# Optimization experiments

Measured on AMD Instinct MI355X. Metric: run time of the kernel, lower is better.

Reference implementation:

```python
import jax, jax.numpy as jnp
import numpy as np

B, H, W = 8, 56, 56
DIM_IN = 1792 + 2   # concatenated pyramid channels + 2 coord channels
D_OUT = 1792 // 4   # gamma_d = 4
N_CENTERS = H * W   # gamma_c = 1
K = 3


def avg_pool3(x):
    # F.avg_pool2d(x, 3, 1, 1) with count_include_pad=True: padded sum / 9
    s = jax.lax.reduce_window(x, 0.0, jax.lax.add, (1, 1, 3, 3), (1, 1, 1, 1),
                              ((0, 0), (0, 0), (1, 1), (1, 1)))
    return s / 9.0


def setup_inputs() -> dict:
    key = jax.random.key(0)
    k0, k1, k2, kw, kb, kc = jax.random.split(key, 6)
    p0 = jax.random.normal(k0, (B, 256, H, W), dtype=jnp.float32)
    p1 = jax.random.normal(k1, (B, 512, 28, 28), dtype=jnp.float32)
    p2 = jax.random.normal(k2, (B, 1024, 14, 14), dtype=jnp.float32)
    conv_w = jax.random.normal(kw, (D_OUT, DIM_IN), dtype=jnp.float32) * 0.02
    conv_b = jax.random.normal(kb, (D_OUT,), dtype=jnp.float32) * 0.01
    C = jax.random.normal(kc, (D_OUT, N_CENTERS), dtype=jnp.float32) * 0.5
    return {"p0": p0, "p1": p1, "p2": p2, "conv_w": conv_w, "conv_b": conv_b, "C": C}


def reference(p0, p1, p2, conv_w, conv_b, C):
    # Descriptor: avg-pool each level, upsample to first level, concat channels
    o0 = avg_pool3(p0)
    o1 = avg_pool3(p1)
    o2 = avg_pool3(p2)
    o1 = jax.image.resize(o1, (B, o1.shape[1], H, W), method='bilinear')  # align_corners=False equiv (upsample)
    o2 = jax.image.resize(o2, (B, o2.shape[1], H, W), method='bilinear')
    sample = jnp.concatenate([o0, o1, o2], axis=1)  # (B, 1792, H, W)

    # AddCoords: xx = row index / (H-1), yy = col index / (W-1), both *2-1
    xx = (jnp.arange(H, dtype=jnp.float32) / (H - 1) * 2 - 1)[:, None] * jnp.ones((1, W), jnp.float32)
    yy = (jnp.arange(W, dtype=jnp.float32) / (W - 1) * 2 - 1)[None, :] * jnp.ones((H, 1), jnp.float32)
    coords = jnp.broadcast_to(jnp.stack([xx, yy])[None], (B, 2, H, W))
    sample = jnp.concatenate([sample, coords], axis=1)  # (B, 1794, H, W)

    # 1x1 CoordConv
    phi = jnp.einsum('bchw,oc->bohw', sample, conv_w) + conv_b[None, :, None, None]
    phi_p = phi.transpose(0, 2, 3, 1).reshape(B, H * W, D_OUT)  # b (h w) c

    # squared distance to center bank via norm expansion
    feat2 = jnp.sum(phi_p ** 2, axis=2, keepdims=True)        # (B, HW, 1)
    cent2 = jnp.sum(C ** 2, axis=0)[None, None, :]            # (1, 1, N)
    dist = jnp.sqrt(feat2 + cent2 - 2.0 * jnp.matmul(phi_p, C))  # (B, HW, N)

    # top-K smallest, ascending
    neg_top, _ = jax.lax.top_k(-dist, K)
    topv = -neg_top                                           # (B, HW, K) ascending
    soft = jax.nn.softmax(-topv, axis=-1)                     # softmin
    score = soft[:, :, 0] * topv[:, :, 0]                     # (B, HW)
    return score.reshape(B, 1, H, W)
```

## Files before the change

kernel.cpp:

```cpp
#include <hip/hip_runtime.h>
#include <math.h>

#define B_    8
#define H_    56
#define W_    56
#define HW_   3136
#define C0_   256
#define C1_   512
#define C2_   1024
#define DIN_  1794
#define KD_   1792
#define KCP_  56
#define DOUT_ 448
#define NCHP_ 28
#define NC_   3136
#define NCHD_ 196
#define KCD_  14
#define DTS_  452
#define PCH_  28672

typedef __attribute__((ext_vector_type(8))) short bh8;
typedef __attribute__((ext_vector_type(4))) float f32x4;

__device__ __forceinline__ short f2bf(float f) {
  union { float f; unsigned u; } v; v.f = f;
  unsigned r = v.u + 0x7fffu + ((v.u >> 16) & 1u);
  return (short)(r >> 16);
}
__device__ __forceinline__ float bf2f(short s) {
  union { unsigned u; float f; } v; v.u = ((unsigned)(unsigned short)s) << 16;
  return v.f;
}

__global__ __launch_bounds__(256) void desc0_kernel(const float* __restrict__ p0,
                                                    short* __restrict__ desc) {
  __shared__ float sv[64 * 57];
  const int c0 = blockIdx.x * 64, h = blockIdx.y, b = blockIdx.z;
  for (int item = threadIdx.x; item < 64 * 56; item += 256) {
    int x = item % 56, c = item / 56;
    const float* src = p0 + (((size_t)(b * C0_ + c0 + c)) * 56 + h) * 56 + x;
    float s = src[0];
    if (h > 0)  s += src[-56];
    if (h < 55) s += src[56];
    sv[c * 57 + x] = s;
  }
  __syncthreads();
  for (int item = threadIdx.x; item < 56 * 8; item += 256) {
    int g = item & 7, w = item >> 3;
    bh8 o;
#pragma unroll
    for (int j = 0; j < 8; ++j) {
      const float* s0 = sv + (g * 8 + j) * 57;
      float v = s0[w];
      if (w > 0)  v += s0[w - 1];
      if (w < 55) v += s0[w + 1];
      o[j] = f2bf(v * (1.0f / 9.0f));
    }
    size_t pid = (size_t)b * HW_ + h * 56 + w;
    *(bh8*)(desc + pid * KD_ + c0 + g * 8) = o;
  }
}

__global__ __launch_bounds__(256) void desc1_kernel(const float* __restrict__ p1,
                                                    short* __restrict__ desc) {
  __shared__ float sv[2 * 64 * 29];
  const int c0 = blockIdx.x * 64, h = blockIdx.y, b = blockIdx.z;
  float sy = (h + 0.5f) * 0.5f - 0.5f;
  float fyf = floorf(sy);
  float fy = sy - fyf;
  int iy = (int)fyf;
  int pya = min(max(iy, 0), 27), pyb = min(max(iy + 1, 0), 27);
  for (int item = threadIdx.x; item < 64 * 2 * 28; item += 256) {
    int x = item % 28;
    int pr = (item / 28) & 1;
    int c = item / 56;
    int r = pr ? pyb : pya;
    const float* src = p1 + (((size_t)(b * C1_ + c0 + c)) * 28 + r) * 28 + x;
    float s = src[0];
    if (r > 0)  s += src[-28];
    if (r < 27) s += src[28];
    sv[pr * (64 * 29) + c * 29 + x] = s;
  }
  __syncthreads();
  for (int item = threadIdx.x; item < 56 * 8; item += 256) {
    int g = item & 7, w = item >> 3;
    float sx = (w + 0.5f) * 0.5f - 0.5f;
    float fxf = floorf(sx);
    float fx = sx - fxf;
    int ix = (int)fxf;
    int x0 = min(max(ix, 0), 27), x1 = min(max(ix + 1, 0), 27);
    bh8 o;
#pragma unroll
    for (int j = 0; j < 8; ++j) {
      const float* s0 = sv + (g * 8 + j) * 29;
      const float* s1 = s0 + 64 * 29;
      float p00 = s0[x0] + (x0 > 0 ? s0[x0 - 1] : 0.f) + (x0 < 27 ? s0[x0 + 1] : 0.f);
      float p01 = s0[x1] + (x1 > 0 ? s0[x1 - 1] : 0.f) + (x1 < 27 ? s0[x1 + 1] : 0.f);
      float p10 = s1[x0] + (x0 > 0 ? s1[x0 - 1] : 0.f) + (x0 < 27 ? s1[x0 + 1] : 0.f);
      float p11 = s1[x1] + (x1 > 0 ? s1[x1 - 1] : 0.f) + (x1 < 27 ? s1[x1 + 1] : 0.f);
      float top = p00 + fx * (p01 - p00);
      float bot = p10 + fx * (p11 - p10);
      o[j] = f2bf((top + fy * (bot - top)) * (1.0f / 9.0f));
    }
    size_t pid = (size_t)b * HW_ + h * 56 + w;
    *(bh8*)(desc + pid * KD_ + C0_ + c0 + g * 8) = o;
  }
}

__global__ __launch_bounds__(256) void desc2_kernel(const float* __restrict__ p2,
                                                    short* __restrict__ desc) {
  __shared__ float sv[2 * 64 * 15];
  const int c0 = blockIdx.x * 64, h = blockIdx.y, b = blockIdx.z;
  float sy = (h + 0.5f) * 0.25f - 0.5f;
  float fyf = floorf(sy);
  float fy = sy - fyf;
  int iy = (int)fyf;
  int pya = min(max(iy, 0), 13), pyb = min(max(iy + 1, 0), 13);
  for (int item = threadIdx.x; item < 64 * 2 * 14; item += 256) {
    int x = item % 14;
    int pr = (item / 14) & 1;
    int c = item / 28;
    int r = pr ? pyb : pya;
    const float* src = p2 + (((size_t)(b * C2_ + c0 + c)) * 14 + r) * 14 + x;
    float s = src[0];
    if (r > 0)  s += src[-14];
    if (r < 13) s += src[14];
    sv[pr * (64 * 15) + c * 15 + x] = s;
  }
  __syncthreads();
  for (int item = threadIdx.x; item < 56 * 8; item += 256) {
    int g = item & 7, w = item >> 3;
    float sx = (w + 0.5f) * 0.25f - 0.5f;
    float fxf = floorf(sx);
    float fx = sx - fxf;
    int ix = (int)fxf;
    int x0 = min(max(ix, 0), 13), x1 = min(max(ix + 1, 0), 13);
    bh8 o;
#pragma unroll
    for (int j = 0; j < 8; ++j) {
      const float* s0 = sv + (g * 8 + j) * 15;
      const float* s1 = s0 + 64 * 15;
      float p00 = s0[x0] + (x0 > 0 ? s0[x0 - 1] : 0.f) + (x0 < 13 ? s0[x0 + 1] : 0.f);
      float p01 = s0[x1] + (x1 > 0 ? s0[x1 - 1] : 0.f) + (x1 < 13 ? s0[x1 + 1] : 0.f);
      float p10 = s1[x0] + (x0 > 0 ? s1[x0 - 1] : 0.f) + (x0 < 13 ? s1[x0 + 1] : 0.f);
      float p11 = s1[x1] + (x1 > 0 ? s1[x1 - 1] : 0.f) + (x1 < 13 ? s1[x1 + 1] : 0.f);
      float top = p00 + fx * (p01 - p00);
      float bot = p10 + fx * (p11 - p10);
      o[j] = f2bf((top + fy * (bot - top)) * (1.0f / 9.0f));
    }
    size_t pid = (size_t)b * HW_ + h * 56 + w;
    *(bh8*)(desc + pid * KD_ + C0_ + C1_ + c0 + g * 8) = o;
  }
}

__global__ void cent2_kernel(const float* __restrict__ C, float* __restrict__ c2) {
  int j = blockIdx.x * blockDim.x + threadIdx.x;
  if (j >= NC_) return;
  float s = 0.f;
  for (int d = 0; d < DOUT_; ++d) {
    float v = bf2f(f2bf(C[(size_t)d * NC_ + j]));
    s = fmaf(v, v, s);
  }
  c2[j] = s;
}

__global__ void cpack_kernel(const float* __restrict__ C, short* __restrict__ Cpk) {
  int idx = blockIdx.x * 256 + threadIdx.x;
  int ln = idx & 63;
  int kc = (idx >> 6) % KCD_;
  int nc = idx / (KCD_ * 64);
  int n  = nc * 16 + (ln & 15);
  int k0 = kc * 32 + ((ln >> 4) << 3);
  bh8 o;
#pragma unroll
  for (int j = 0; j < 8; ++j) o[j] = f2bf(C[(size_t)(k0 + j) * NC_ + n]);
  *(bh8*)(Cpk + (size_t)idx * 8) = o;
}

__global__ void wpack_kernel(const float* __restrict__ W, short* __restrict__ Wpk) {
  int idx = blockIdx.x * 256 + threadIdx.x;
  int ln = idx & 63;
  int kc = (idx >> 6) % KCP_;
  int nc = idx / (KCP_ * 64);
  int n  = nc * 16 + (ln & 15);
  int k0 = kc * 32 + ((ln >> 4) << 3);
  bh8 o;
#pragma unroll
  for (int j = 0; j < 8; ++j) o[j] = f2bf(W[(size_t)n * DIN_ + k0 + j]);
  *(bh8*)(Wpk + (size_t)idx * 8) = o;
}

__global__ __launch_bounds__(256) void phi_mfma(
    const short* __restrict__ desc, const short* __restrict__ Wpk,
    const float* __restrict__ cw, const float* __restrict__ cb,
    short* __restrict__ phip ) {
  __shared__ __align__(16) float Dt[16 * DTS_];
  const int wv = threadIdx.x >> 6, ln = threadIdx.x & 63;
  const int pix0 = blockIdx.x * 32;
  const short* aptr = desc + ((size_t)(pix0 + (ln & 15))) * KD_ + ((ln >> 4) << 3);

  f32x4 acc[2][7];
#pragma unroll
  for (int rc = 0; rc < 2; ++rc)
#pragma unroll
    for (int i = 0; i < 7; ++i) acc[rc][i] = (f32x4){0.f, 0.f, 0.f, 0.f};

  const short* bbase = Wpk + (size_t)(wv * 7) * (KCP_ * 512) + ln * 8;
  for (int kc = 0; kc < KCP_; ++kc) {
    bh8 a0 = *(const bh8*)(aptr + kc * 32);
    bh8 a1 = *(const bh8*)(aptr + 16 * KD_ + kc * 32);
    const short* bp = bbase + kc * 512;
#pragma unroll
    for (int i = 0; i < 7; ++i) {
      bh8 bfr = *(const bh8*)(bp + (size_t)i * (KCP_ * 512));
      acc[0][i] = __builtin_amdgcn_mfma_f32_16x16x32_bf16(a0, bfr, acc[0][i], 0, 0, 0);
      acc[1][i] = __builtin_amdgcn_mfma_f32_16x16x32_bf16(a1, bfr, acc[1][i], 0, 0, 0);
    }
  }

  for (int rc = 0; rc < 2; ++rc) {
    __syncthreads();
#pragma unroll
    for (int i = 0; i < 7; ++i) {
      int col = (wv * 7 + i) * 16 + (ln & 15);
      float bias = cb[col];
      float wx = cw[(size_t)col * DIN_ + 1792];
      float wy = cw[(size_t)col * DIN_ + 1793];
#pragma unroll
      for (int r = 0; r < 4; ++r) {
        int row = ((ln >> 4) << 2) + r;
        int pid = pix0 + rc * 16 + row;
        int hw = pid % HW_;
        int hh = hw / 56, ww = hw % 56;
        float xx = (float)hh * (2.0f / 55.0f) - 1.0f;
        float yy = (float)ww * (2.0f / 55.0f) - 1.0f;
        Dt[row * DTS_ + col] = acc[rc][i][r] + bias + wx * xx + wy * yy;
      }
    }
    __syncthreads();
    short* op = phip + (size_t)(blockIdx.x * 2 + rc) * PCH_;
    for (int item = threadIdx.x; item < KCD_ * 64; item += 256) {
      int kc = item >> 6, lp = item & 63;
      int m = lp & 15, k0 = kc * 32 + ((lp >> 4) << 3);
      bh8 o;
#pragma unroll
      for (int j = 0; j < 8; ++j) o[j] = f2bf(Dt[m * DTS_ + k0 + j]);
      *(bh8*)(op + (size_t)item * 8) = o;
    }
  }
}

__device__ __forceinline__ void insert3(float& t0, float& t1, float& t2, float v) {
  if (v < t2) {
    if (v < t1) {
      t2 = t1;
      if (v < t0) { t1 = t0; t0 = v; } else t1 = v;
    } else t2 = v;
  }
}
__device__ __forceinline__ void merge3(float& a0, float& a1, float& a2,
                                       float b0, float b1, float b2) {
  float lo0 = fminf(a0, b0), hi0 = fmaxf(a0, b0);
  float lo1 = fminf(a1, b1), hi1 = fmaxf(a1, b1);
  float lo2 = fminf(a2, b2);
  a0 = lo0;
  a1 = fminf(hi0, lo1);
  a2 = fminf(fmaxf(hi0, lo1), fminf(hi1, lo2));
}
__device__ __forceinline__ float sumsq8(bh8 a, float s) {
#pragma unroll
  for (int j = 0; j < 8; ++j) { float v = bf2f(a[j]); s = fmaf(v, v, s); }
  return s;
}

#define AFRAG_LIST(X) X(0) X(1) X(2) X(3) X(4) X(5) X(6) X(7) X(8) X(9) X(10) X(11) X(12) X(13)

__global__ __launch_bounds__(256, 2) void dist_part(
    const short* __restrict__ phip, const short* __restrict__ Cpk,
    const float* __restrict__ c2g, float* __restrict__ part) {
  __shared__ __align__(16) short Bst[2][14336];
  __shared__ float c2l[NC_ / 2];
  const int wv = threadIdx.x >> 6, ln = threadIdx.x & 63;
  const int half = blockIdx.x & 1;
  const int chunk = (blockIdx.x >> 1) * 4 + wv;

  for (int i = threadIdx.x; i < NC_ / 2; i += 256) c2l[i] = c2g[half * (NC_ / 2) + i];

  const short* ap = phip + (size_t)chunk * PCH_ + ln * 8;
#define LOADA(i) bh8 A##i = *(const bh8*)(ap + (i) * 512);
  AFRAG_LIST(LOADA)
#undef LOADA

  float sum = 0.f;
#define SQ(i) sum = sumsq8(A##i, sum);
  AFRAG_LIST(SQ)
#undef SQ
  sum += __shfl_xor(sum, 16, 64);
  sum += __shfl_xor(sum, 32, 64);
  const int rb = (ln >> 4) << 2;
  float f2r0 = __shfl(sum, rb + 0, 64);
  float f2r1 = __shfl(sum, rb + 1, 64);
  float f2r2 = __shfl(sum, rb + 2, 64);
  float f2r3 = __shfl(sum, rb + 3, 64);

  float t00 = 1e30f, t01 = 1e30f, t02 = 1e30f;
  float t10 = 1e30f, t11 = 1e30f, t12 = 1e30f;
  float t20 = 1e30f, t21 = 1e30f, t22 = 1e30f;
  float t30 = 1e30f, t31 = 1e30f, t32 = 1e30f;

  const int col = ln & 15;
  const short* cbase = Cpk + (size_t)half * ((NCHD_ / 2) * KCD_ * 512);

#define STAGE(buf, t) { \
    const short* g_ = cbase + (size_t)(t) * 14336 + wv * 3584 + ln * 8; \
    short* l_ = &Bst[(buf)][wv * 3584]; \
    _Pragma("unroll") \
    for (int j_ = 0; j_ < 7; ++j_) \
      __builtin_amdgcn_global_load_lds( \
          (const __attribute__((address_space(1))) unsigned int*)(g_ + j_ * 512), \
          (__attribute__((address_space(3))) unsigned int*)(l_ + j_ * 512), \
          16, 0, 0); }

  STAGE(0, 0)
  __syncthreads();

  for (int t = 0; t < NCHD_ / 4; ++t) {
    if (t < NCHD_ / 4 - 1) STAGE((t + 1) & 1, t + 1)
    const short* bp = &Bst[t & 1][ln * 8];
    f32x4 accA = {0.f, 0.f, 0.f, 0.f}, accB = {0.f, 0.f, 0.f, 0.f};
#define MF(kc) { \
    bh8 bA = *(const bh8*)(bp + (kc) * 512); \
    bh8 bB = *(const bh8*)(bp + 7168 + (kc) * 512); \
    accA = __builtin_amdgcn_mfma_f32_16x16x32_bf16(A##kc, bA, accA, 0, 0, 0); \
    accB = __builtin_amdgcn_mfma_f32_16x16x32_bf16(A##kc, bB, accB, 0, 0, 0); }
    AFRAG_LIST(MF)
#undef MF
    float c2A = c2l[t * 32 + col];
    float c2B = c2l[t * 32 + 16 + col];
    insert3(t00, t01, t02, f2r0 + c2A - 2.0f * accA[0]);
    insert3(t10, t11, t12, f2r1 + c2A - 2.0f * accA[1]);
    insert3(t20, t21, t22, f2r2 + c2A - 2.0f * accA[2]);
    insert3(t30, t31, t32, f2r3 + c2A - 2.0f * accA[3]);
    insert3(t00, t01, t02, f2r0 + c2B - 2.0f * accB[0]);
    insert3(t10, t11, t12, f2r1 + c2B - 2.0f * accB[1]);
    insert3(t20, t21, t22, f2r2 + c2B - 2.0f * accB[2]);
    insert3(t30, t31, t32, f2r3 + c2B - 2.0f * accB[3]);
    __syncthreads();
  }
#undef STAGE

#pragma unroll
  for (int m = 1; m <= 8; m <<= 1) {
    float b0, b1, b2;
    b0 = __shfl_xor(t00, m, 64); b1 = __shfl_xor(t01, m, 64); b2 = __shfl_xor(t02, m, 64);
    merge3(t00, t01, t02, b0, b1, b2);
    b0 = __shfl_xor(t10, m, 64); b1 = __shfl_xor(t11, m, 64); b2 = __shfl_xor(t12, m, 64);
    merge3(t10, t11, t12, b0, b1, b2);
    b0 = __shfl_xor(t20, m, 64); b1 = __shfl_xor(t21, m, 64); b2 = __shfl_xor(t22, m, 64);
    merge3(t20, t21, t22, b0, b1, b2);
    b0 = __shfl_xor(t30, m, 64); b1 = __shfl_xor(t31, m, 64); b2 = __shfl_xor(t32, m, 64);
    merge3(t30, t31, t32, b0, b1, b2);
  }

  if ((ln & 15) == 0) {
    float* q = part + ((size_t)(chunk * 16 + rb)) * 8 + half * 4;
    q[0] = t00; q[1] = t01; q[2] = t02;
    q[8] = t10; q[9] = t11; q[10] = t12;
    q[16] = t20; q[17] = t21; q[18] = t22;
    q[24] = t30; q[25] = t31; q[26] = t32;
  }
}

__global__ __launch_bounds__(256) void merge_kernel(const float* __restrict__ part,
                                                    float* __restrict__ out) {
  int p = blockIdx.x * 256 + threadIdx.x;
  const float* q = part + (size_t)p * 8;
  float a0 = q[0], a1 = q[1], a2 = q[2];
  merge3(a0, a1, a2, q[4], q[5], q[6]);
  float d0 = sqrtf(fmaxf(a0, 0.f));
  float d1 = sqrtf(fmaxf(a1, 0.f));
  float d2 = sqrtf(fmaxf(a2, 0.f));
  float s0 = 1.0f / (1.0f + expf(d0 - d1) + expf(d0 - d2));
  out[p] = s0 * d0;
}

extern "C" void kernel_launch(void* const* d_in, const int* in_sizes, int n_in,
                              void* d_out, int out_size, void* d_ws, size_t ws_size,
                              hipStream_t stream) {
  const float* p0 = (const float*)d_in[0];
  const float* p1 = (const float*)d_in[1];
  const float* p2 = (const float*)d_in[2];
  const float* cw = (const float*)d_in[3];
  const float* cb = (const float*)d_in[4];
  const float* C  = (const float*)d_in[5];
  float* out = (float*)d_out;

  short* desc = (short*)d_ws;
  short* Cpk  = desc + (size_t)25088 * KD_;
  short* Wpk  = Cpk + (size_t)NCHD_ * KCD_ * 512;
  float* c2   = (float*)(Wpk + (size_t)NCHP_ * KCP_ * 512);
  float* part = c2 + NC_;

  desc0_kernel<<<dim3(4, 56, 8),  256, 0, stream>>>(p0, desc);
  desc1_kernel<<<dim3(8, 56, 8),  256, 0, stream>>>(p1, desc);
  desc2_kernel<<<dim3(16, 56, 8), 256, 0, stream>>>(p2, desc);
  cent2_kernel<<<(NC_ + 255) / 256, 256, 0, stream>>>(C, c2);
  cpack_kernel<<<NCHD_ * KCD_ * 64 / 256, 256, 0, stream>>>(C, Cpk);
  wpack_kernel<<<NCHP_ * KCP_ * 64 / 256, 256, 0, stream>>>(cw, Wpk);
  phi_mfma<<<25088 / 32, 256, 0, stream>>>(desc, Wpk, cw, cb, desc);
  dist_part<<<784, 256, 0, stream>>>(desc, Cpk, c2, part);
  merge_kernel<<<25088 / 256, 256, 0, stream>>>(part, out);
}
```

Before: 721.8 us.

## Process two row chunks per wave in dist_part to reuse staged centre fragments

Each wave now keeps A fragments for two 16-row chunks in registers and runs both against every B fragment loaded from LDS, so each LDS read of the centre tile feeds two MFMAs. The grid is halved to 392 blocks, so global-to-LDS staging of the centre bank is spread over half as many blocks. In exchange, register pressure roughly doubles for the A fragments and the top-3 state, which can hurt occupancy under launch_bounds(256,2). Having fewer blocks than before also risks leaving compute units underfilled.

```diff
diff --git a/kernel.cpp b/kernel.cpp
--- a/kernel.cpp
+++ b/kernel.cpp
@@ -273,7 +273,7 @@
   return s;
 }
 
-#define AFRAG_LIST(X) X(0) X(1) X(2) X(3) X(4) X(5) X(6) X(7) X(8) X(9) X(10) X(11) X(12) X(13)
+#define KLIST(X) X(0) X(1) X(2) X(3) X(4) X(5) X(6) X(7) X(8) X(9) X(10) X(11) X(12) X(13)
 
 __global__ __launch_bounds__(256, 2) void dist_part(
     const short* __restrict__ phip, const short* __restrict__ Cpk,
@@ -282,31 +282,39 @@
   __shared__ float c2l[NC_ / 2];
   const int wv = threadIdx.x >> 6, ln = threadIdx.x & 63;
   const int half = blockIdx.x & 1;
-  const int chunk = (blockIdx.x >> 1) * 4 + wv;
+  const int chunk = (blockIdx.x >> 1) * 8 + wv * 2;
 
   for (int i = threadIdx.x; i < NC_ / 2; i += 256) c2l[i] = c2g[half * (NC_ / 2) + i];
 
-  const short* ap = phip + (size_t)chunk * PCH_ + ln * 8;
-#define LOADA(i) bh8 A##i = *(const bh8*)(ap + (i) * 512);
-  AFRAG_LIST(LOADA)
+  const short* ap0 = phip + (size_t)chunk * PCH_ + ln * 8;
+  const short* ap1 = ap0 + PCH_;
+#define LOADA(i) bh8 A##i = *(const bh8*)(ap0 + (i) * 512); \
+                 bh8 T##i = *(const bh8*)(ap1 + (i) * 512);
+  KLIST(LOADA)
 #undef LOADA
 
-  float sum = 0.f;
-#define SQ(i) sum = sumsq8(A##i, sum);
-  AFRAG_LIST(SQ)
+  float s0 = 0.f, s1 = 0.f;
+#define SQ(i) s0 = sumsq8(A##i, s0); s1 = sumsq8(T##i, s1);
+  KLIST(SQ)
 #undef SQ
-  sum += __shfl_xor(sum, 16, 64);
-  sum += __shfl_xor(sum, 32, 64);
+  s0 += __shfl_xor(s0, 16, 64);
+  s0 += __shfl_xor(s0, 32, 64);
+  s1 += __shfl_xor(s1, 16, 64);
+  s1 += __shfl_xor(s1, 32, 64);
   const int rb = (ln >> 4) << 2;
-  float f2r0 = __shfl(sum, rb + 0, 64);
-  float f2r1 = __shfl(sum, rb + 1, 64);
-  float f2r2 = __shfl(sum, rb + 2, 64);
-  float f2r3 = __shfl(sum, rb + 3, 64);
+  float f2a0 = __shfl(s0, rb + 0, 64), f2a1 = __shfl(s0, rb + 1, 64);
+  float f2a2 = __shfl(s0, rb + 2, 64), f2a3 = __shfl(s0, rb + 3, 64);
+  float f2b0 = __shfl(s1, rb + 0, 64), f2b1 = __shfl(s1, rb + 1, 64);
+  float f2b2 = __shfl(s1, rb + 2, 64), f2b3 = __shfl(s1, rb + 3, 64);
 
   float t00 = 1e30f, t01 = 1e30f, t02 = 1e30f;
   float t10 = 1e30f, t11 = 1e30f, t12 = 1e30f;
   float t20 = 1e30f, t21 = 1e30f, t22 = 1e30f;
   float t30 = 1e30f, t31 = 1e30f, t32 = 1e30f;
+  float u00 = 1e30f, u01 = 1e30f, u02 = 1e30f;
+  float u10 = 1e30f, u11 = 1e30f, u12 = 1e30f;
+  float u20 = 1e30f, u21 = 1e30f, u22 = 1e30f;
+  float u30 = 1e30f, u31 = 1e30f, u32 = 1e30f;
 
   const int col = ln & 15;
   const short* cbase = Cpk + (size_t)half * ((NCHD_ / 2) * KCD_ * 512);
@@ -326,25 +334,45 @@
 
   for (int t = 0; t < NCHD_ / 4; ++t) {
     if (t < NCHD_ / 4 - 1) STAGE((t + 1) & 1, t + 1)
-    const short* bp = &Bst[t & 1][ln * 8];
-    f32x4 accA = {0.f, 0.f, 0.f, 0.f}, accB = {0.f, 0.f, 0.f, 0.f};
-#define MF(kc) { \
-    bh8 bA = *(const bh8*)(bp + (kc) * 512); \
-    bh8 bB = *(const bh8*)(bp + 7168 + (kc) * 512); \
-    accA = __builtin_amdgcn_mfma_f32_16x16x32_bf16(A##kc, bA, accA, 0, 0, 0); \
-    accB = __builtin_amdgcn_mfma_f32_16x16x32_bf16(A##kc, bB, accB, 0, 0, 0); }
-    AFRAG_LIST(MF)
-#undef MF
-    float c2A = c2l[t * 32 + col];
-    float c2B = c2l[t * 32 + 16 + col];
-    insert3(t00, t01, t02, f2r0 + c2A - 2.0f * accA[0]);
-    insert3(t10, t11, t12, f2r1 + c2A - 2.0f * accA[1]);
-    insert3(t20, t21, t22, f2r2 + c2A - 2.0f * accA[2]);
-    insert3(t30, t31, t32, f2r3 + c2A - 2.0f * accA[3]);
-    insert3(t00, t01, t02, f2r0 + c2B - 2.0f * accB[0]);
-    insert3(t10, t11, t12, f2r1 + c2B - 2.0f * accB[1]);
-    insert3(t20, t21, t22, f2r2 + c2B - 2.0f * accB[2]);
-    insert3(t30, t31, t32, f2r3 + c2B - 2.0f * accB[3]);
+    const short* bq = &Bst[t & 1][ln * 8];
+    {
+      f32x4 accP = {0.f, 0.f, 0.f, 0.f}, accQ = {0.f, 0.f, 0.f, 0.f};
+#define LB(kc) bh8 B##kc = *(const bh8*)(bq + (kc) * 512);
+      KLIST(LB)
+#undef LB
+#define MF2(kc) accP = __builtin_amdgcn_mfma_f32_16x16x32_bf16(A##kc, B##kc, accP, 0, 0, 0); \
+                accQ = __builtin_amdgcn_mfma_f32_16x16x32_bf16(T##kc, B##kc, accQ, 0, 0, 0);
+      KLIST(MF2)
+#undef MF2
+      float c2A = c2l[t * 32 + col];
+      insert3(t00, t01, t02, f2a0 + c2A - 2.0f * accP[0]);
+      insert3(t10, t11, t12, f2a1 + c2A - 2.0f * accP[1]);
+      insert3(t20, t21, t22, f2a2 + c2A - 2.0f * accP[2]);
+      insert3(t30, t31, t32, f2a3 + c2A - 2.0f * accP[3]);
+      insert3(u00, u01, u02, f2b0 + c2A - 2.0f * accQ[0]);
+      insert3(u10, u11, u12, f2b1 + c2A - 2.0f * accQ[1]);
+      insert3(u20, u21, u22, f2b2 + c2A - 2.0f * accQ[2]);
+      insert3(u30, u31, u32, f2b3 + c2A - 2.0f * accQ[3]);
+    }
+    {
+      f32x4 accP = {0.f, 0.f, 0.f, 0.f}, accQ = {0.f, 0.f, 0.f, 0.f};
+#define LB(kc) bh8 B##kc = *(const bh8*)(bq + 7168 + (kc) * 512);
+      KLIST(LB)
+#undef LB
+#define MF2(kc) accP = __builtin_amdgcn_mfma_f32_16x16x32_bf16(A##kc, B##kc, accP, 0, 0, 0); \
+                accQ = __builtin_amdgcn_mfma_f32_16x16x32_bf16(T##kc, B##kc, accQ, 0, 0, 0);
+      KLIST(MF2)
+#undef MF2
+      float c2B = c2l[t * 32 + 16 + col];
+      insert3(t00, t01, t02, f2a0 + c2B - 2.0f * accP[0]);
+      insert3(t10, t11, t12, f2a1 + c2B - 2.0f * accP[1]);
+      insert3(t20, t21, t22, f2a2 + c2B - 2.0f * accP[2]);
+      insert3(t30, t31, t32, f2a3 + c2B - 2.0f * accP[3]);
+      insert3(u00, u01, u02, f2b0 + c2B - 2.0f * accQ[0]);
+      insert3(u10, u11, u12, f2b1 + c2B - 2.0f * accQ[1]);
+      insert3(u20, u21, u22, f2b2 + c2B - 2.0f * accQ[2]);
+      insert3(u30, u31, u32, f2b3 + c2B - 2.0f * accQ[3]);
+    }
     __syncthreads();
   }
 #undef STAGE
@@ -360,6 +388,14 @@
     merge3(t20, t21, t22, b0, b1, b2);
     b0 = __shfl_xor(t30, m, 64); b1 = __shfl_xor(t31, m, 64); b2 = __shfl_xor(t32, m, 64);
     merge3(t30, t31, t32, b0, b1, b2);
+    b0 = __shfl_xor(u00, m, 64); b1 = __shfl_xor(u01, m, 64); b2 = __shfl_xor(u02, m, 64);
+    merge3(u00, u01, u02, b0, b1, b2);
+    b0 = __shfl_xor(u10, m, 64); b1 = __shfl_xor(u11, m, 64); b2 = __shfl_xor(u12, m, 64);
+    merge3(u10, u11, u12, b0, b1, b2);
+    b0 = __shfl_xor(u20, m, 64); b1 = __shfl_xor(u21, m, 64); b2 = __shfl_xor(u22, m, 64);
+    merge3(u20, u21, u22, b0, b1, b2);
+    b0 = __shfl_xor(u30, m, 64); b1 = __shfl_xor(u31, m, 64); b2 = __shfl_xor(u32, m, 64);
+    merge3(u30, u31, u32, b0, b1, b2);
   }
 
   if ((ln & 15) == 0) {
@@ -368,6 +404,11 @@
     q[8] = t10; q[9] = t11; q[10] = t12;
     q[16] = t20; q[17] = t21; q[18] = t22;
     q[24] = t30; q[25] = t31; q[26] = t32;
+    float* r = part + ((size_t)((chunk + 1) * 16 + rb)) * 8 + half * 4;
+    r[0] = u00; r[1] = u01; r[2] = u02;
+    r[8] = u10; r[9] = u11; r[10] = u12;
+    r[16] = u20; r[17] = u21; r[18] = u22;
+    r[24] = u30; r[25] = u31; r[26] = u32;
   }
 }
 
@@ -408,6 +449,6 @@
   cpack_kernel<<<NCHD_ * KCD_ * 64 / 256, 256, 0, stream>>>(C, Cpk);
   wpack_kernel<<<NCHP_ * KCP_ * 64 / 256, 256, 0, stream>>>(cw, Wpk);
   phi_mfma<<<25088 / 32, 256, 0, stream>>>(desc, Wpk, cw, cb, desc);
-  dist_part<<<784, 256, 0, stream>>>(desc, Cpk, c2, part);
+  dist_part<<<392, 256, 0, stream>>>(desc, Cpk, c2, part);
   merge_kernel<<<25088 / 256, 256, 0, stream>>>(part, out);
 }
```

New measurement: 701.9 us. 1.03x faster.
